# Performance work log

Hardware: AMD Instinct MI355X
Metric: run time of the kernel (lower is better)

## Reference

```python
import jax, jax.numpy as jnp
import numpy as np

D_MODEL = 128
NUM_HEAD = 4
HEAD_DIM = D_MODEL // NUM_HEAD
VOCAB = 32000
MAX_LEN = 4096


def _positional_encoding(max_len, d_model):
    i = jnp.arange(d_model // 2, dtype=jnp.float32)
    pos = jnp.arange(max_len, dtype=jnp.float32)[:, None]
    angle = pos / 10000.0 ** (2.0 * i / d_model)  # [max_len, d_model/2]
    pe = jnp.zeros((max_len, d_model), dtype=jnp.float32)
    pe = pe.at[:, ::2].set(jnp.sin(angle))
    pe = pe.at[:, 1::2].set(jnp.cos(angle))
    return pe  # [max_len, d_model]


def setup_inputs() -> dict:
    key = jax.random.key(0)
    k0, k1, k2, k3, k4, k5 = jax.random.split(key, 6)
    B, S = 2, 4096
    scale = 1.0 / np.sqrt(D_MODEL)
    return {
        "input_seq": jax.random.randint(k0, (B, S), 0, VOCAB, dtype=jnp.int32),
        "embedding": jax.random.normal(k1, (VOCAB, D_MODEL), dtype=jnp.float32),
        "w_q": jax.random.normal(k2, (D_MODEL, D_MODEL), dtype=jnp.float32) * scale,
        "w_k": jax.random.normal(k3, (D_MODEL, D_MODEL), dtype=jnp.float32) * scale,
        "w_v": jax.random.normal(k4, (D_MODEL, D_MODEL), dtype=jnp.float32) * scale,
        "w_o": jax.random.normal(k5, (D_MODEL, D_MODEL), dtype=jnp.float32) * scale,
    }


def reference(input_seq, embedding, w_q, w_k, w_v, w_o):
    B, S = input_seq.shape
    x = embedding[input_seq]  # [B, S, D]
    pe = _positional_encoding(MAX_LEN, D_MODEL)[:S]  # [S, D]
    x = x + pe[None, :, :]
    # torch Linear (no bias): y = x @ W.T
    q = jnp.einsum('bsd,ed->bse', x, w_q)
    k = jnp.einsum('bsd,ed->bse', x, w_k)
    v = jnp.einsum('bsd,ed->bse', x, w_v)
    # faithful to original: plain view (no transpose) splitting into heads
    q = q.reshape(B, NUM_HEAD, S, HEAD_DIM)
    k = k.reshape(B, NUM_HEAD, S, HEAD_DIM)
    v = v.reshape(B, NUM_HEAD, S, HEAD_DIM)
    raw = jnp.einsum('bhqd,bhkd->bhqk', q, k) / np.sqrt(HEAD_DIM)
    # custom abs * tril(-inf) masking
    tril = jnp.tril(jnp.ones((S, S), dtype=raw.dtype))
    masked = jnp.where(tril == 0, -jnp.inf, 1.0).astype(raw.dtype)
    raw = jnp.abs(raw) * masked
    attn = jax.nn.softmax(raw, axis=-1)
    out = jnp.einsum('bhqk,bhkd->bhqd', attn, v)
    out = out.reshape(B, S, D_MODEL)  # faithful plain view
    return jnp.einsum('bsd,ed->bse', out, w_o)
```

## Files before the change

### kernel.cpp

```cpp
#include <hip/hip_runtime.h>
#include <hip/hip_bf16.h>
#include <cmath>

#define D_MODEL 128
#define NUM_HEAD 4
#define HEAD_DIM 32
#define SEQ 4096
#define BATCH 2
#define RROWS 8
#define QROWS 16

typedef __attribute__((ext_vector_type(8))) short short8;
typedef __attribute__((ext_vector_type(4))) float f32x4;

__device__ __forceinline__ float tof(float x) { return x; }
__device__ __forceinline__ float tof(__hip_bfloat16 x) { return __bfloat162float(x); }
__device__ __forceinline__ void storef(float* p, size_t i, float v) { p[i] = v; }
__device__ __forceinline__ void storef(__hip_bfloat16* p, size_t i, float v) { p[i] = __float2bfloat16(v); }

__device__ __forceinline__ void split_bf16(float x, unsigned short& hi, unsigned short& lo)
{
    const unsigned u = __float_as_uint(x);
    const unsigned r = u + 0x7FFFu + ((u >> 16) & 1u);
    hi = (unsigned short)(r >> 16);
    const float hf = __uint_as_float((unsigned)hi << 16);
    const float lf = x - hf;
    const unsigned ul = __float_as_uint(lf);
    const unsigned rl = ul + 0x7FFFu + ((ul >> 16) & 1u);
    lo = (unsigned short)(rl >> 16);
}
__device__ __forceinline__ unsigned short rne_bf16(float x)
{
    const unsigned u = __float_as_uint(x);
    return (unsigned short)((u + 0x7FFFu + ((u >> 16) & 1u)) >> 16);
}

__device__ __forceinline__ void g2l16(const void* g, void* l)
{
    __builtin_amdgcn_global_load_lds(
        (const __attribute__((address_space(1))) void*)g,
        (__attribute__((address_space(3))) void*)l, 16, 0, 0);
}

__global__ __launch_bounds__(256) void prep_kernel(
    const void* wq, const void* wk, const void* wv, const void* wo,
    float* __restrict__ wt4, float* __restrict__ pe, int* __restrict__ flagp)
{
    const int bx  = blockIdx.x;
    const int tid = threadIdx.x;
    __shared__ int sflag;

    if (bx < 64) {
        {
            int weird = 0;
            if (tid < 64) {
                const unsigned short* w16 = (const unsigned short*)wq;
#pragma unroll
                for (int j = 0; j < 4; ++j) {
                    const unsigned short v = w16[(tid * 4 + j) * 2 + 1];
                    const float x = __uint_as_float((unsigned)v << 16);
                    const float a = fabsf(x);
                    if (a > 1e20f || (a > 0.f && a < 1e-20f)) weird++;
                }
#pragma unroll
                for (int off = 32; off; off >>= 1) weird += __shfl_xor(weird, off);
                if (tid == 0) sflag = (weird < 32) ? 1 : 0;
            }
            __syncthreads();
        }
        const int flag = sflag;
        if (bx == 0 && tid == 0) *flagp = flag;

        const int m = bx >> 4;
        const void* w = (m == 0) ? wq : (m == 1) ? wk : (m == 2) ? wv : wo;
        const int item = (bx & 15) * 256 + tid;
        const int e  = item & 127;
        const int dq = item >> 7;
        float4 v;
        if (flag) {
            v = *(const float4*)((const float*)w + (size_t)e * 128 + dq * 4);
        } else {
            const __hip_bfloat16* wb = (const __hip_bfloat16*)w + (size_t)e * 128 + dq * 4;
            v = make_float4(tof(wb[0]), tof(wb[1]), tof(wb[2]), tof(wb[3]));
        }
        *(float4*)&wt4[(((size_t)m * 32 + dq) * 128 + e) * 4] = v;
    } else {
        const int idx   = (bx - 64) * 256 + tid;
        const int i     = idx & 63;
        const int chunk = idx >> 6;
        const int s0    = chunk * 128;
        const double inv = 1.0 / pow(10000.0, (double)i / 64.0);
        const double a0  = (double)s0 * inv;
        double c  = cos(a0), s = sin(a0);
        const double cd = cos(inv), sd = sin(inv);
        float2* row = (float2*)&pe[(size_t)s0 * 128 + i * 2];
        for (int k = 0; k < 128; ++k) {
            float2 sc;
            sc.x = (float)s;
            sc.y = (float)c;
            row[(size_t)k * 64] = sc;
            const double cn = c * cd - s * sd;
            s = s * cd + c * sd;
            c = cn;
        }
    }
}

template <typename T>
__device__ __forceinline__ void qkv_body(
    const int* __restrict__ seq, const T* __restrict__ emb,
    const float* __restrict__ wt4, const float* __restrict__ pe,
    unsigned short* __restrict__ Qhi, unsigned short* __restrict__ Qlo,
    unsigned short* __restrict__ Khi, unsigned short* __restrict__ Klo,
    unsigned short* __restrict__ Vthi, unsigned short* __restrict__ Vtlo)
{
    const int tid = threadIdx.x;
    const int e   = tid & 127;
    const int grp = tid >> 7;
    const int r0  = blockIdx.x * QROWS;

    __shared__ __align__(16) float xs[QROWS][D_MODEL];
    __shared__ __align__(16) unsigned short vsh[2][QROWS][D_MODEL];

#pragma unroll
    for (int k = 0; k < 4; ++k) {
        const int idx = k * 512 + tid;
        const int r  = idx >> 7;
        const int ee = idx & 127;
        const int srow = r0 + r;
        xs[r][ee] = tof(emb[(size_t)seq[srow] * D_MODEL + ee])
                  + pe[(size_t)(srow & (SEQ - 1)) * D_MODEL + ee];
    }
    __syncthreads();

    float aq[4], ak[4], av[4];
#pragma unroll
    for (int r = 0; r < 4; ++r) { aq[r] = 0.f; ak[r] = 0.f; av[r] = 0.f; }

    const int rbase = grp * 4;
    const float4* wq4 = (const float4*)wt4;
    const float4* wk4 = wq4 + 4096;
    const float4* wv4 = wq4 + 8192;

    for (int dq = 0; dq < 32; ++dq) {
        float4 xr[4];
#pragma unroll
        for (int r = 0; r < 4; ++r) xr[r] = *(const float4*)&xs[rbase + r][dq * 4];
        const float4 wq_ = wq4[dq * 128 + e];
        const float4 wk_ = wk4[dq * 128 + e];
        const float4 wv_ = wv4[dq * 128 + e];
#pragma unroll
        for (int r = 0; r < 4; ++r) {
            aq[r] += xr[r].x * wq_.x; aq[r] += xr[r].y * wq_.y;
            aq[r] += xr[r].z * wq_.z; aq[r] += xr[r].w * wq_.w;
            ak[r] += xr[r].x * wk_.x; ak[r] += xr[r].y * wk_.y;
            ak[r] += xr[r].z * wk_.z; ak[r] += xr[r].w * wk_.w;
            av[r] += xr[r].x * wv_.x; av[r] += xr[r].y * wv_.y;
            av[r] += xr[r].z * wv_.z; av[r] += xr[r].w * wv_.w;
        }
    }

    const float scale = 0.17677669529663687f;
#pragma unroll
    for (int r = 0; r < 4; ++r) {
        const int row = rbase + r;
        const size_t o = (size_t)(r0 + row) * D_MODEL + e;
        unsigned short hi, lo;
        split_bf16(aq[r] * scale, hi, lo); Qhi[o] = hi; Qlo[o] = lo;
        split_bf16(ak[r], hi, lo);         Khi[o] = hi; Klo[o] = lo;
        split_bf16(av[r], hi, lo);         vsh[0][row][e] = hi; vsh[1][row][e] = lo;
    }
    __syncthreads();

    {
        const int b  = r0 >> 12;
        const int s0 = r0 & (SEQ - 1);
        const int h  = s0 >> 10;
        const size_t vtb = (size_t)(b * 4 + h) * (32 * SEQ);
        const int hl = tid >> 8;
        const int d  = (tid >> 3) & 31;
        const int j  = tid & 7;
        short8 tmp;
#pragma unroll
        for (int i = 0; i < 8; ++i) {
            const int kl = j * 8 + i;
            tmp[i] = (short)vsh[hl][kl >> 2][(kl & 3) * 32 + d];
        }
        unsigned short* dst = (hl ? Vtlo : Vthi) + vtb + (size_t)d * SEQ
                            + (size_t)(s0 & 1023) * 4 + j * 8;
        *(short8*)dst = tmp;
    }
}

__global__ __launch_bounds__(512, 4) void qkv_kernel(
    const int* __restrict__ seq, const void* emb,
    const float* __restrict__ wt4, const float* __restrict__ pe,
    unsigned short* Qhi, unsigned short* Qlo,
    unsigned short* Khi, unsigned short* Klo,
    unsigned short* Vthi, unsigned short* Vtlo,
    const int* __restrict__ flag)
{
    if (*flag)
        qkv_body<float>(seq, (const float*)emb, wt4, pe,
                        Qhi, Qlo, Khi, Klo, Vthi, Vtlo);
    else
        qkv_body<__hip_bfloat16>(seq, (const __hip_bfloat16*)emb, wt4, pe,
                                 Qhi, Qlo, Khi, Klo, Vthi, Vtlo);
}

__global__ __launch_bounds__(256, 4) void attn_kernel(
    const unsigned short* __restrict__ Qhi, const unsigned short* __restrict__ Qlo,
    const unsigned short* __restrict__ Khi, const unsigned short* __restrict__ Klo,
    const unsigned short* __restrict__ Vthi, const unsigned short* __restrict__ Vtlo,
    float* __restrict__ Apart, float* __restrict__ lbuf)
{
    const int bh   = blockIdx.x;
    const int by   = blockIdx.y;
    const int kh   = blockIdx.z;
    const int qt   = (by < 32) ? by : 95 - by;
    const size_t baseQ  = (size_t)(bh >> 2) * SEQ * D_MODEL + (size_t)(bh & 3) * SEQ * HEAD_DIM;
    const size_t baseVt = (size_t)bh * (32 * SEQ);

    const int tid  = threadIdx.x;
    const int wid  = __builtin_amdgcn_readfirstlane(tid >> 6);
    const int lane = tid & 63;
    const int rt   = wid;
    const int quad = lane >> 4;
    const int col  = lane & 15;

    __shared__ float shbuf[4 * 576];
    __shared__ __align__(16) unsigned char kv[3][8192];
    float* pb = &shbuf[wid * 576];

    const int qrow0 = qt * 64 + rt * 16;

    short8 qhiF, qloF;
    {
        const size_t qo = baseQ + (size_t)(qrow0 + col) * HEAD_DIM + quad * 8;
        qhiF = *(const short8*)(Qhi + qo);
        qloF = *(const short8*)(Qlo + qo);
    }

    f32x4 O0 = {0.f, 0.f, 0.f, 0.f};
    f32x4 O1 = {0.f, 0.f, 0.f, 0.f};
    float l[4] = {0.f, 0.f, 0.f, 0.f};

    const int N   = 2 * (qt + 1);
    const int nb  = N >> 2, rem = N & 3;
    const int cnt  = nb + ((kh < rem) ? 1 : 0);
    const int cbeg = kh * nb + ((kh < rem) ? kh : rem);

    const int r4 = lane >> 2, sseg = lane & 3;
    auto stage = [&](int bufi, int kbase) {
#pragma unroll
        for (int half = 0; half < 2; ++half) {
            const int row = half * 16 + r4;
            const int seg = sseg ^ (row & 3);
            const unsigned short* src;
            if (wid == 0)      src = Khi  + baseQ  + (size_t)(kbase + row) * HEAD_DIM + seg * 8;
            else if (wid == 1) src = Klo  + baseQ  + (size_t)(kbase + row) * HEAD_DIM + seg * 8;
            else if (wid == 2) src = Vthi + baseVt + (size_t)row * SEQ + kbase + seg * 8;
            else               src = Vtlo + baseVt + (size_t)row * SEQ + kbase + seg * 8;
            g2l16(src, &kv[bufi][wid * 2048 + half * 1024]);
        }
    };
    auto frag = [&](int bufi, int plane, int row) -> short8 {
        const int byte = plane * 2048 + row * 64 + ((quad ^ (row & 3)) << 4);
        return *(const short8*)(&kv[bufi][byte]);
    };

    if (cnt > 0) {
        stage(0, cbeg * 32);
        if (cnt > 1) stage(1, (cbeg + 1) * 32);
        int cur = 0;
        for (int i = 0; i < cnt; ++i) {
            const int c = cbeg + i;
            const int kbase = c * 32;
            if (i + 1 < cnt) { asm volatile("s_waitcnt vmcnt(2)" ::: "memory"); }
            else             { asm volatile("s_waitcnt vmcnt(0)" ::: "memory"); }
            __builtin_amdgcn_s_barrier();
            __builtin_amdgcn_sched_barrier(0);
            if (i + 2 < cnt) {
                int nx = cur + 2; if (nx > 2) nx -= 3;
                stage(nx, (c + 2) * 32);
            }

            const short8 k0h = frag(cur, 0, col);
            const short8 k0l = frag(cur, 1, col);
            const short8 k1h = frag(cur, 0, col + 16);
            const short8 k1l = frag(cur, 1, col + 16);

            f32x4 s0v = {0.f, 0.f, 0.f, 0.f};
            f32x4 s1v = {0.f, 0.f, 0.f, 0.f};
            s0v = __builtin_amdgcn_mfma_f32_16x16x32_bf16(qhiF, k0h, s0v, 0, 0, 0);
            s0v = __builtin_amdgcn_mfma_f32_16x16x32_bf16(qhiF, k0l, s0v, 0, 0, 0);
            s0v = __builtin_amdgcn_mfma_f32_16x16x32_bf16(qloF, k0h, s0v, 0, 0, 0);
            s1v = __builtin_amdgcn_mfma_f32_16x16x32_bf16(qhiF, k1h, s1v, 0, 0, 0);
            s1v = __builtin_amdgcn_mfma_f32_16x16x32_bf16(qhiF, k1l, s1v, 0, 0, 0);
            s1v = __builtin_amdgcn_mfma_f32_16x16x32_bf16(qloF, k1h, s1v, 0, 0, 0);

#pragma unroll
            for (int r = 0; r < 4; ++r) {
                const int rowg = qrow0 + quad * 4 + r;
                const float e0 = (kbase + col      <= rowg) ? __expf(fabsf(s0v[r])) : 0.f;
                const float e1 = (kbase + 16 + col <= rowg) ? __expf(fabsf(s1v[r])) : 0.f;
                l[r] += e0 + e1;
                pb[(quad * 4 + r) * 36 + col]      = e0;
                pb[(quad * 4 + r) * 36 + 16 + col] = e1;
            }
            short8 ph;
            {
                const float4 p01 = *(const float4*)&pb[col * 36 + quad * 8];
                const float4 p23 = *(const float4*)&pb[col * 36 + quad * 8 + 4];
                ph[0] = (short)rne_bf16(p01.x); ph[1] = (short)rne_bf16(p01.y);
                ph[2] = (short)rne_bf16(p01.z); ph[3] = (short)rne_bf16(p01.w);
                ph[4] = (short)rne_bf16(p23.x); ph[5] = (short)rne_bf16(p23.y);
                ph[6] = (short)rne_bf16(p23.z); ph[7] = (short)rne_bf16(p23.w);
            }

            const short8 v0h = frag(cur, 2, col);
            const short8 v0l = frag(cur, 3, col);
            const short8 v1h = frag(cur, 2, col + 16);
            const short8 v1l = frag(cur, 3, col + 16);

            O0 = __builtin_amdgcn_mfma_f32_16x16x32_bf16(ph, v0h, O0, 0, 0, 0);
            O0 = __builtin_amdgcn_mfma_f32_16x16x32_bf16(ph, v0l, O0, 0, 0, 0);
            O1 = __builtin_amdgcn_mfma_f32_16x16x32_bf16(ph, v1h, O1, 0, 0, 0);
            O1 = __builtin_amdgcn_mfma_f32_16x16x32_bf16(ph, v1l, O1, 0, 0, 0);

            cur = (cur == 2) ? 0 : cur + 1;
        }
    }

#pragma unroll
    for (int off = 1; off < 16; off <<= 1) {
#pragma unroll
        for (int r = 0; r < 4; ++r) l[r] += __shfl_xor(l[r], off, 64);
    }

    float* Ap = Apart + (size_t)kh * (BATCH * SEQ * D_MODEL) + baseQ;
#pragma unroll
    for (int r = 0; r < 4; ++r) {
        const int row = qrow0 + quad * 4 + r;
        Ap[(size_t)row * HEAD_DIM + col]      = O0[r];
        Ap[(size_t)row * HEAD_DIM + 16 + col] = O1[r];
    }
    if (col == 0) {
        float* lp = lbuf + ((size_t)kh * (BATCH * NUM_HEAD) + bh) * SEQ;
#pragma unroll
        for (int r = 0; r < 4; ++r)
            lp[qrow0 + quad * 4 + r] = l[r];
    }
}

template <typename T>
__device__ __forceinline__ void out_proj_body(
    const float* __restrict__ Apart, const float* __restrict__ lbuf,
    const float* __restrict__ wo4t, T* __restrict__ out)
{
    const int tid = threadIdx.x;
    const int e   = tid & 127;
    const int grp = tid >> 7;
    const int r0  = blockIdx.x * RROWS;

    __shared__ __align__(16) float xs[RROWS][D_MODEL];
#pragma unroll
    for (int k = 0; k < 4; ++k) {
        const int idx = k * 256 + tid;
        const int rr = idx >> 7;
        const int ee = idx & 127;
        const int gr = r0 + rr;
        const int b  = gr >> 12;
        const int s  = gr & (SEQ - 1);
        const int bh = b * 4 + (s >> 10);
        const int hr = ((s & 1023) << 2) + (ee >> 5);
        const size_t ai = (size_t)gr * D_MODEL + ee;
        float sum = 0.f, Ls = 0.f;
#pragma unroll
        for (int kh = 0; kh < 4; ++kh) {
            sum += Apart[(size_t)kh * (BATCH * SEQ * D_MODEL) + ai];
            Ls  += lbuf[((size_t)kh * (BATCH * NUM_HEAD) + bh) * SEQ + hr];
        }
        xs[rr][ee] = sum * (1.f / Ls);
    }
    __syncthreads();

    float acc[4] = {0.f, 0.f, 0.f, 0.f};
    const int rbase = grp * 4;
    const float4* w4 = (const float4*)wo4t;

    for (int dq = 0; dq < 32; ++dq) {
        float4 xr[4];
#pragma unroll
        for (int r = 0; r < 4; ++r) xr[r] = *(const float4*)&xs[rbase + r][dq * 4];
        const float4 w_ = w4[dq * 128 + e];
#pragma unroll
        for (int r = 0; r < 4; ++r) {
            acc[r] += xr[r].x * w_.x; acc[r] += xr[r].y * w_.y;
            acc[r] += xr[r].z * w_.z; acc[r] += xr[r].w * w_.w;
        }
    }
#pragma unroll
    for (int r = 0; r < 4; ++r)
        storef(out, (size_t)(r0 + rbase + r) * D_MODEL + e, acc[r]);
}

__global__ __launch_bounds__(256, 4) void out_proj_kernel(
    const float* __restrict__ Apart, const float* __restrict__ lbuf,
    const float* __restrict__ wo4t, void* out,
    const int* __restrict__ flag)
{
    if (*flag)
        out_proj_body<float>(Apart, lbuf, wo4t, (float*)out);
    else
        out_proj_body<__hip_bfloat16>(Apart, lbuf, wo4t, (__hip_bfloat16*)out);
}

extern "C" void kernel_launch(void* const* d_in, const int* in_sizes, int n_in,
                              void* d_out, int out_size, void* d_ws, size_t ws_size,
                              hipStream_t stream) {
    const int* seq = (const int*)d_in[0];
    const void* emb = d_in[1];
    const void* wq  = d_in[2];
    const void* wk  = d_in[3];
    const void* wv  = d_in[4];
    const void* wo  = d_in[5];

    const size_t N = (size_t)BATCH * SEQ * D_MODEL;
    int*            flag = (int*)d_ws;
    unsigned short* Qhi  = (unsigned short*)((char*)d_ws + 256);
    unsigned short* Qlo  = Qhi + N;
    unsigned short* Khi  = Qlo + N;
    unsigned short* Klo  = Khi + N;
    unsigned short* Vthi = Klo + N;
    unsigned short* Vtlo = Vthi + N;
    float*          Apart = (float*)(Vtlo + N);
    float*          lbuf  = Apart + 4 * N;
    float*          wt4   = lbuf + 4 * BATCH * NUM_HEAD * SEQ;
    float*          pe    = wt4 + 65536;

    prep_kernel<<<dim3(64 + 8), dim3(256), 0, stream>>>(wq, wk, wv, wo, wt4, pe, flag);
    qkv_kernel<<<dim3(BATCH * SEQ / QROWS), dim3(512), 0, stream>>>(
        seq, emb, wt4, pe,
        Qhi, Qlo, Khi, Klo, Vthi, Vtlo, flag);
    attn_kernel<<<dim3(BATCH * NUM_HEAD, 64, 4), dim3(256), 0, stream>>>(
        Qhi, Qlo, Khi, Klo, Vthi, Vtlo, Apart, lbuf);
    out_proj_kernel<<<dim3(BATCH * SEQ / RROWS), dim3(256), 0, stream>>>(
        Apart, lbuf, wt4 + 49152, d_out, flag);
}
```

Before: 160.2 us.

## Split QKV projection over input-dim quarters with shared-memory reduction

The QKV projection kernel changes its work split. Each of the four thread groups now covers one quarter of the input dimension for all 16 rows, instead of covering 4 rows over the full dimension. Partial sums are reduced through a new 32KB shared-memory buffer in three passes, one each for Q, K and V. The aim is to cut redundant weight loads, since each weight float4 is now read once per block instead of once per group. In exchange it uses 48 accumulators, adds extra barriers and shared traffic, and halves the occupancy hint.

```diff
diff --git a/kernel.cpp b/kernel.cpp
--- a/kernel.cpp
+++ b/kernel.cpp
@@ -121,6 +121,7 @@
 
     __shared__ __align__(16) float xs[QROWS][D_MODEL];
     __shared__ __align__(16) unsigned short vsh[2][QROWS][D_MODEL];
+    __shared__ __align__(16) float red[4][QROWS][D_MODEL];
 
 #pragma unroll
     for (int k = 0; k < 4; ++k) {
@@ -133,42 +134,70 @@
     }
     __syncthreads();
 
-    float aq[4], ak[4], av[4];
-#pragma unroll
-    for (int r = 0; r < 4; ++r) { aq[r] = 0.f; ak[r] = 0.f; av[r] = 0.f; }
-
-    const int rbase = grp * 4;
+    float aq[QROWS], ak[QROWS], av[QROWS];
+#pragma unroll
+    for (int r = 0; r < QROWS; ++r) { aq[r] = 0.f; ak[r] = 0.f; av[r] = 0.f; }
+
     const float4* wq4 = (const float4*)wt4;
     const float4* wk4 = wq4 + 4096;
     const float4* wv4 = wq4 + 8192;
 
-    for (int dq = 0; dq < 32; ++dq) {
-        float4 xr[4];
-#pragma unroll
-        for (int r = 0; r < 4; ++r) xr[r] = *(const float4*)&xs[rbase + r][dq * 4];
+    const int dqb = grp * 8;
+    for (int j = 0; j < 8; ++j) {
+        const int dq = dqb + j;
         const float4 wq_ = wq4[dq * 128 + e];
         const float4 wk_ = wk4[dq * 128 + e];
         const float4 wv_ = wv4[dq * 128 + e];
 #pragma unroll
-        for (int r = 0; r < 4; ++r) {
-            aq[r] += xr[r].x * wq_.x; aq[r] += xr[r].y * wq_.y;
-            aq[r] += xr[r].z * wq_.z; aq[r] += xr[r].w * wq_.w;
-            ak[r] += xr[r].x * wk_.x; ak[r] += xr[r].y * wk_.y;
-            ak[r] += xr[r].z * wk_.z; ak[r] += xr[r].w * wk_.w;
-            av[r] += xr[r].x * wv_.x; av[r] += xr[r].y * wv_.y;
-            av[r] += xr[r].z * wv_.z; av[r] += xr[r].w * wv_.w;
-        }
-    }
-
+        for (int r = 0; r < QROWS; ++r) {
+            const float4 x = *(const float4*)&xs[r][dq * 4];
+            aq[r] += x.x * wq_.x; aq[r] += x.y * wq_.y;
+            aq[r] += x.z * wq_.z; aq[r] += x.w * wq_.w;
+            ak[r] += x.x * wk_.x; ak[r] += x.y * wk_.y;
+            ak[r] += x.z * wk_.z; ak[r] += x.w * wk_.w;
+            av[r] += x.x * wv_.x; av[r] += x.y * wv_.y;
+            av[r] += x.z * wv_.z; av[r] += x.w * wv_.w;
+        }
+    }
+
+    const int rbase = grp * 4;
     const float scale = 0.17677669529663687f;
+
+    __syncthreads();
+#pragma unroll
+    for (int r = 0; r < QROWS; ++r) red[grp][r][e] = aq[r];
+    __syncthreads();
 #pragma unroll
     for (int r = 0; r < 4; ++r) {
         const int row = rbase + r;
+        const float v = ((red[0][row][e] + red[1][row][e]) + red[2][row][e]) + red[3][row][e];
         const size_t o = (size_t)(r0 + row) * D_MODEL + e;
         unsigned short hi, lo;
-        split_bf16(aq[r] * scale, hi, lo); Qhi[o] = hi; Qlo[o] = lo;
-        split_bf16(ak[r], hi, lo);         Khi[o] = hi; Klo[o] = lo;
-        split_bf16(av[r], hi, lo);         vsh[0][row][e] = hi; vsh[1][row][e] = lo;
+        split_bf16(v * scale, hi, lo); Qhi[o] = hi; Qlo[o] = lo;
+    }
+    __syncthreads();
+#pragma unroll
+    for (int r = 0; r < QROWS; ++r) red[grp][r][e] = ak[r];
+    __syncthreads();
+#pragma unroll
+    for (int r = 0; r < 4; ++r) {
+        const int row = rbase + r;
+        const float v = ((red[0][row][e] + red[1][row][e]) + red[2][row][e]) + red[3][row][e];
+        const size_t o = (size_t)(r0 + row) * D_MODEL + e;
+        unsigned short hi, lo;
+        split_bf16(v, hi, lo); Khi[o] = hi; Klo[o] = lo;
+    }
+    __syncthreads();
+#pragma unroll
+    for (int r = 0; r < QROWS; ++r) red[grp][r][e] = av[r];
+    __syncthreads();
+#pragma unroll
+    for (int r = 0; r < 4; ++r) {
+        const int row = rbase + r;
+        const float v = ((red[0][row][e] + red[1][row][e]) + red[2][row][e]) + red[3][row][e];
+        unsigned short hi, lo;
+        split_bf16(v, hi, lo);
+        vsh[0][row][e] = hi; vsh[1][row][e] = lo;
     }
     __syncthreads();
 
@@ -192,7 +221,7 @@
     }
 }
 
-__global__ __launch_bounds__(512, 4) void qkv_kernel(
+__global__ __launch_bounds__(512, 2) void qkv_kernel(
     const int* __restrict__ seq, const void* emb,
     const float* __restrict__ wt4, const float* __restrict__ pe,
     unsigned short* Qhi, unsigned short* Qlo,
```

Measured after the change: 162.5 us. About the same (+1.4%).
